# Kernel tuning notes

Measured on AMD Instinct MI355X. Metric: run time of the kernel, lower is better.

## Reference

```python
import jax, jax.numpy as jnp
import numpy as np

B, T, I, H, O, F = 256, 2048, 64, 256, 64, 16
NUM_LAYERS = 2


def setup_inputs() -> dict:
    key = jax.random.key(0)
    ks = jax.random.split(key, 12)
    s = 1.0 / np.sqrt(H)  # PyTorch RNN/Linear init scale
    u = lambda k, shp: jax.random.uniform(k, shp, jnp.float32, -s, s)
    return {
        "x": jax.random.normal(ks[0], (B, T, I), jnp.float32),
        "hidden": jnp.zeros((NUM_LAYERS, B, H), jnp.float32),
        "W_ih0": u(ks[1], (H, I)),
        "W_hh0": u(ks[2], (H, H)),
        "b_ih0": u(ks[3], (H,)),
        "b_hh0": u(ks[4], (H,)),
        "W_ih1": u(ks[5], (H, H)),
        "W_hh1": u(ks[6], (H, H)),
        "b_ih1": u(ks[7], (H,)),
        "b_hh1": u(ks[8], (H,)),
        "fc_W": u(ks[9], (O, H)),
        "fc_b": u(ks[10], (O,)),
        "future_timesegments": F,
    }


def _rnn_layer(xs, h0, W_ih, W_hh, b_ih, b_hh):
    # xs: [T, B, in_dim]; h0: [B, H]
    # Precompute input contribution for all timesteps (one big GEMM),
    # then scan only the sequential recurrence h@W_hh^T + tanh.
    pre = jnp.einsum('tbi,hi->tbh', xs, W_ih) + b_ih + b_hh  # [T, B, H]

    def step(h, p_t):
        h_new = jnp.tanh(p_t + h @ W_hh.T)
        return h_new, h_new

    h_T, ys = jax.lax.scan(step, h0, pre)
    return ys, h_T  # ys: [T, B, H]


def reference(x, hidden, W_ih0, W_hh0, b_ih0, b_hh0,
              W_ih1, W_hh1, b_ih1, b_hh1, fc_W, fc_b,
              future_timesegments):
    xs = jnp.swapaxes(x, 0, 1)  # [T, B, I] (batch_first -> time major)
    ys0, h0 = _rnn_layer(xs, hidden[0], W_ih0, W_hh0, b_ih0, b_hh0)
    ys1, h1 = _rnn_layer(ys0, hidden[1], W_ih1, W_hh1, b_ih1, b_hh1)
    # out[:, -F:, :] in batch-first layout
    tail = jnp.swapaxes(ys1[-future_timesegments:], 0, 1)  # [B, F, H]
    out = tail @ fc_W.T + fc_b  # [B, F, O]
    new_hidden = jnp.stack([h0, h1])  # [num_layers, B, H]
    return out, new_hidden
```

## Files before the change

### kernel.cpp

```cpp
#include <hip/hip_runtime.h>

#define BB 256
#define TT 2048
#define II 64
#define HH 256
#define OO 64
#define FF 16


#define BUFSZ 1280
#define BUF0 0
#define BUF1 BUFSZ
#define H1OFF 576
#define XOFF 1152
#define HSL 144
#define XSL 32
#define TAILOFF (2 * BUFSZ)
#define LDSBYTES (TAILOFF + FF * HH * 2)

typedef _Float16 h8 __attribute__((ext_vector_type(8)));

__device__ __forceinline__ void adot(float& acc, int hv, int wv) {
  asm("v_dot2_f32_f16 %0, %1, %2, %0" : "+v"(acc) : "v"(hv), "v"(wv));
}

__device__ __forceinline__ float fast_tanh(float z) {
  float e = __builtin_amdgcn_exp2f(z * 2.885390081777927f);
  return 1.0f - 2.0f * __builtin_amdgcn_rcpf(e + 1.0f);
}

__device__ __forceinline__ int pk2i(const float* p) {
  union { _Float16 h[2]; int i; } u;
  u.h[0] = (_Float16)p[0]; u.h[1] = (_Float16)p[1];
  return u.i;
}

template <int CTRL>
__device__ __forceinline__ float dpp_add(float v) {
  union { float f; int i; } a, r;
  a.f = v;
  r.i = __builtin_amdgcn_update_dpp(0, a.i, CTRL, 0xF, 0xF, true);
  return v + r.f;
}

#define RNN_STEP(T, RB, WB)                                                    \
  {                                                                            \
    float xn = 0.f;                                                            \
    if ((tid & 7) == 0) {                                                      \
      int tn = (T) + 1 < TT ? (T) + 1 : (T);                                   \
      xn = xrow[(size_t)tn * II + xi];                                         \
    }                                                                          \
    float a00 = 0.f, a01 = 0.f, a10 = 0.f, a11 = 0.f;                          \
    _Pragma("unroll") for (int c = 0; c < 2; ++c) {                            \
      const int4 v = *(const int4*)(xaddr + (RB) + c * 16);                    \
      adot(a00, v.x, w0x[0][4 * c + 0]); adot(a00, v.y, w0x[0][4 * c + 1]);    \
      adot(a00, v.z, w0x[0][4 * c + 2]); adot(a00, v.w, w0x[0][4 * c + 3]);    \
      adot(a01, v.x, w0x[1][4 * c + 0]); adot(a01, v.y, w0x[1][4 * c + 1]);    \
      adot(a01, v.z, w0x[1][4 * c + 2]); adot(a01, v.w, w0x[1][4 * c + 3]);    \
    }                                                                          \
    _Pragma("unroll") for (int c = 0; c < 8; ++c) {                            \
      const int4 v = *(const int4*)(h0addr + (RB) + c * 16);                   \
      adot(a00, v.x, w0h[0][4 * c + 0]); adot(a00, v.y, w0h[0][4 * c + 1]);    \
      adot(a00, v.z, w0h[0][4 * c + 2]); adot(a00, v.w, w0h[0][4 * c + 3]);    \
      adot(a01, v.x, w0h[1][4 * c + 0]); adot(a01, v.y, w0h[1][4 * c + 1]);    \
      adot(a01, v.z, w0h[1][4 * c + 2]); adot(a01, v.w, w0h[1][4 * c + 3]);    \
      adot(a10, v.x, w1g[0][4 * c + 0]); adot(a10, v.y, w1g[0][4 * c + 1]);    \
      adot(a10, v.z, w1g[0][4 * c + 2]); adot(a10, v.w, w1g[0][4 * c + 3]);    \
      adot(a11, v.x, w1g[1][4 * c + 0]); adot(a11, v.y, w1g[1][4 * c + 1]);    \
      adot(a11, v.z, w1g[1][4 * c + 2]); adot(a11, v.w, w1g[1][4 * c + 3]);    \
    }                                                                          \
    _Pragma("unroll") for (int c = 0; c < 8; ++c) {                            \
      const int4 v = *(const int4*)(h0addr + (RB) + H1OFF + c * 16);           \
      adot(a10, v.x, w1h[0][4 * c + 0]); adot(a10, v.y, w1h[0][4 * c + 1]);    \
      adot(a10, v.z, w1h[0][4 * c + 2]); adot(a10, v.w, w1h[0][4 * c + 3]);    \
      adot(a11, v.x, w1h[1][4 * c + 0]); adot(a11, v.y, w1h[1][4 * c + 1]);    \
      adot(a11, v.z, w1h[1][4 * c + 2]); adot(a11, v.w, w1h[1][4 * c + 3]);    \
    }                                                                          \
    a00 = dpp_add<0xB1>(a00); a00 = dpp_add<0x4E>(a00);                        \
    a01 = dpp_add<0xB1>(a01); a01 = dpp_add<0x4E>(a01);                        \
    a10 = dpp_add<0xB1>(a10); a10 = dpp_add<0x4E>(a10);                        \
    a11 = dpp_add<0xB1>(a11); a11 = dpp_add<0x4E>(a11);                        \
    float v0 = (kg & 1) ? a01 : a00;                                           \
    float v1 = (kg & 1) ? a11 : a10;                                           \
    float hnew = fast_tanh((L ? v1 : v0) + mybias);                            \
    hlast = hnew;                                                              \
    if ((T) > 0 || L == 0) *(_Float16*)(waddr + (WB)) = (_Float16)hnew;        \
    if (L == 1 && (T) >= TT - FF + 1)                                          \
      *(_Float16*)(tailaddr + ((T) - (TT - FF + 1)) * (HH * 2)) =              \
          (_Float16)hnew;                                                      \
    if ((tid & 7) == 0)                                                        \
      *(_Float16*)(lb + (WB) + XOFF + (xi >> 4) * XSL + (xi & 15) * 2) =       \
          (_Float16)xn;                                                        \
    __syncthreads();                                                           \
  }

__global__ __attribute__((amdgpu_flat_work_group_size(512, 512),
                          amdgpu_waves_per_eu(2, 2)))
void rnn_fused(const float* __restrict__ x, const float* __restrict__ hidden,
               const float* __restrict__ Wih0, const float* __restrict__ Whh0,
               const float* __restrict__ bih0, const float* __restrict__ bhh0,
               const float* __restrict__ Wih1, const float* __restrict__ Whh1,
               const float* __restrict__ bih1, const float* __restrict__ bhh1,
               const float* __restrict__ fcW, const float* __restrict__ fcb,
               float* __restrict__ out)
{
  const int tid = threadIdx.x;
  const int b = blockIdx.x;
  const int lane = tid & 63;
  const int kg = lane & 3;
  const int rg = tid >> 2;
  const int j0 = rg * 2;
  const int L = kg >> 1;
  const int cj = j0 + (kg & 1);
  const int xi = tid >> 3;

  __shared__ __align__(16) char lds[LDSBYTES];
  char* lb = (char*)lds;

  int w0x[2][8], w0h[2][32], w1g[2][32], w1h[2][32];
#pragma unroll
  for (int r = 0; r < 2; ++r) {
    const float* p0 = Wih0 + (size_t)(j0 + r) * II + kg * 16;
#pragma unroll
    for (int m = 0; m < 8; ++m) w0x[r][m] = pk2i(p0 + 2 * m);
    const float* p1 = Whh0 + (size_t)(j0 + r) * HH + kg * 64;
#pragma unroll
    for (int m = 0; m < 32; ++m) w0h[r][m] = pk2i(p1 + 2 * m);
    const float* p2 = Wih1 + (size_t)(j0 + r) * HH + kg * 64;
#pragma unroll
    for (int m = 0; m < 32; ++m) w1g[r][m] = pk2i(p2 + 2 * m);
    const float* p3 = Whh1 + (size_t)(j0 + r) * HH + kg * 64;
#pragma unroll
    for (int m = 0; m < 32; ++m) w1h[r][m] = pk2i(p3 + 2 * m);
  }
#pragma unroll
  for (int r = 0; r < 2; ++r) {
#pragma unroll
    for (int m = 0; m < 8; ++m) asm volatile("" : "+v"(w0x[r][m]));
#pragma unroll
    for (int m = 0; m < 32; ++m) {
      asm volatile("" : "+v"(w0h[r][m]));
      asm volatile("" : "+v"(w1g[r][m]));
      asm volatile("" : "+v"(w1h[r][m]));
    }
  }
  float mybias = L ? (bih1[cj] + bhh1[cj]) : (bih0[cj] + bhh0[cj]);
  asm volatile("" : "+v"(mybias));

  const char* h0addr = lb + kg * HSL;
  const char* xaddr = lb + XOFF + kg * XSL;
  char* waddr = lb + (L ? H1OFF : 0) + (cj >> 6) * HSL + (cj & 63) * 2;
  char* tailaddr = lb + TAILOFF + cj * 2;

  if (tid < HH) {
    char* p = lb + (tid >> 6) * HSL + (tid & 63) * 2;
    _Float16 h0v = (_Float16)hidden[(size_t)b * HH + tid];
    _Float16 h1v = (_Float16)hidden[(size_t)(BB + b) * HH + tid];
    *(_Float16*)(p + BUF0) = h0v;
    *(_Float16*)(p + BUF0 + H1OFF) = h1v;
    *(_Float16*)(p + BUF1 + H1OFF) = h1v;
  }
  const float* xrow = x + (size_t)b * TT * II;
  if (tid < II)
    *(_Float16*)(lb + BUF0 + XOFF + (tid >> 4) * XSL + (tid & 15) * 2) =
        (_Float16)xrow[tid];
  float hlast = 0.f, h1last = 0.f;
  __syncthreads();

#pragma unroll 1
  for (int t = 0; t < TT; t += 2) {
    RNN_STEP(t, BUF0, BUF1)
    RNN_STEP(t + 1, BUF1, BUF0)
  }

  {
    float a10 = 0.f, a11 = 0.f;
#pragma unroll
    for (int c = 0; c < 8; ++c) {
      const int4 v = *(const int4*)(h0addr + BUF0 + c * 16);
      adot(a10, v.x, w1g[0][4 * c + 0]); adot(a10, v.y, w1g[0][4 * c + 1]);
      adot(a10, v.z, w1g[0][4 * c + 2]); adot(a10, v.w, w1g[0][4 * c + 3]);
      adot(a11, v.x, w1g[1][4 * c + 0]); adot(a11, v.y, w1g[1][4 * c + 1]);
      adot(a11, v.z, w1g[1][4 * c + 2]); adot(a11, v.w, w1g[1][4 * c + 3]);
    }
#pragma unroll
    for (int c = 0; c < 8; ++c) {
      const int4 v = *(const int4*)(h0addr + BUF0 + H1OFF + c * 16);
      adot(a10, v.x, w1h[0][4 * c + 0]); adot(a10, v.y, w1h[0][4 * c + 1]);
      adot(a10, v.z, w1h[0][4 * c + 2]); adot(a10, v.w, w1h[0][4 * c + 3]);
      adot(a11, v.x, w1h[1][4 * c + 0]); adot(a11, v.y, w1h[1][4 * c + 1]);
      adot(a11, v.z, w1h[1][4 * c + 2]); adot(a11, v.w, w1h[1][4 * c + 3]);
    }
    a10 = dpp_add<0xB1>(a10); a10 = dpp_add<0x4E>(a10);
    a11 = dpp_add<0xB1>(a11); a11 = dpp_add<0x4E>(a11);
    float v1 = (kg & 1) ? a11 : a10;
    float h1e = fast_tanh(v1 + mybias);
    h1last = h1e;
    if (L == 1) *(_Float16*)(tailaddr + (FF - 1) * (HH * 2)) = (_Float16)h1e;
  }
  __syncthreads();

  if (L == 0) out[BB * FF * OO + (size_t)b * HH + cj] = hlast;
  else        out[BB * FF * OO + (size_t)(BB + b) * HH + cj] = h1last;

  const int o = tid & 63;
  const int fg = tid >> 6;
  const _Float16* tp = (const _Float16*)(lb + TAILOFF);
  float acc0 = 0.f, acc1 = 0.f;
  const float* wrow = fcW + o * HH;
  for (int c = 0; c < HH / 8; ++c) {
    float wv[8];
#pragma unroll
    for (int k = 0; k < 8; ++k) wv[k] = wrow[8 * c + k];
    h8 q0 = *(const h8*)(tp + (2 * fg) * HH + 8 * c);
    h8 q1 = *(const h8*)(tp + (2 * fg + 1) * HH + 8 * c);
#pragma unroll
    for (int e = 0; e < 8; ++e) {
      acc0 += (float)q0[e] * wv[e];
      acc1 += (float)q1[e] * wv[e];
    }
  }
  const float bo = fcb[o];
  out[((size_t)b * FF + 2 * fg) * OO + o] = acc0 + bo;
  out[((size_t)b * FF + 2 * fg + 1) * OO + o] = acc1 + bo;
}

extern "C" void kernel_launch(void* const* d_in, const int* in_sizes, int n_in,
                              void* d_out, int out_size, void* d_ws, size_t ws_size,
                              hipStream_t stream) {
  (void)in_sizes; (void)n_in; (void)d_ws; (void)ws_size; (void)out_size;
  rnn_fused<<<dim3(BB), dim3(512), 0, stream>>>(
      (const float*)d_in[0],  (const float*)d_in[1],
      (const float*)d_in[2],  (const float*)d_in[3],
      (const float*)d_in[4],  (const float*)d_in[5],
      (const float*)d_in[6],  (const float*)d_in[7],
      (const float*)d_in[8],  (const float*)d_in[9],
      (const float*)d_in[10], (const float*)d_in[11],
      (float*)d_out);
}
```

Measured before the change: 3.146 ms.

## Split each hidden unit's dot products across eight lanes with 1024-thread blocks

Each row pair is now reduced by eight lanes instead of four, and the block doubles to 1024 threads. This halves the per-thread reduction length and the weight registers, with an extra DPP reduction step added. The intent is to shorten the serial critical path of each recurrence step and allow more waves per SIMD. In exchange, a 1024-thread barrier runs every step, and half the lanes compute redundant tanh values whose results are discarded.

```diff
diff --git a/kernel.cpp b/kernel.cpp
--- a/kernel.cpp
+++ b/kernel.cpp
@@ -8,13 +8,12 @@
 #define FF 16
 
 
-#define BUFSZ 1280
+#define BUFSZ 1408
 #define BUF0 0
 #define BUF1 BUFSZ
-#define H1OFF 576
-#define XOFF 1152
-#define HSL 144
-#define XSL 32
+#define H1OFF 640
+#define XOFF 1280
+#define HSL 80
 #define TAILOFF (2 * BUFSZ)
 #define LDSBYTES (TAILOFF + FF * HH * 2)
 
@@ -46,19 +45,19 @@
 #define RNN_STEP(T, RB, WB)                                                    \
   {                                                                            \
     float xn = 0.f;                                                            \
-    if ((tid & 7) == 0) {                                                      \
+    if ((tid & 15) == 0) {                                                     \
       int tn = (T) + 1 < TT ? (T) + 1 : (T);                                   \
       xn = xrow[(size_t)tn * II + xi];                                         \
     }                                                                          \
     float a00 = 0.f, a01 = 0.f, a10 = 0.f, a11 = 0.f;                          \
-    _Pragma("unroll") for (int c = 0; c < 2; ++c) {                            \
-      const int4 v = *(const int4*)(xaddr + (RB) + c * 16);                    \
-      adot(a00, v.x, w0x[0][4 * c + 0]); adot(a00, v.y, w0x[0][4 * c + 1]);    \
-      adot(a00, v.z, w0x[0][4 * c + 2]); adot(a00, v.w, w0x[0][4 * c + 3]);    \
-      adot(a01, v.x, w0x[1][4 * c + 0]); adot(a01, v.y, w0x[1][4 * c + 1]);    \
-      adot(a01, v.z, w0x[1][4 * c + 2]); adot(a01, v.w, w0x[1][4 * c + 3]);    \
-    }                                                                          \
-    _Pragma("unroll") for (int c = 0; c < 8; ++c) {                            \
+    {                                                                          \
+      const int4 xv = *(const int4*)(xaddr + (RB));                            \
+      adot(a00, xv.x, w0x[0][0]); adot(a00, xv.y, w0x[0][1]);                  \
+      adot(a00, xv.z, w0x[0][2]); adot(a00, xv.w, w0x[0][3]);                  \
+      adot(a01, xv.x, w0x[1][0]); adot(a01, xv.y, w0x[1][1]);                  \
+      adot(a01, xv.z, w0x[1][2]); adot(a01, xv.w, w0x[1][3]);                  \
+    }                                                                          \
+    _Pragma("unroll") for (int c = 0; c < 4; ++c) {                            \
       const int4 v = *(const int4*)(h0addr + (RB) + c * 16);                   \
       adot(a00, v.x, w0h[0][4 * c + 0]); adot(a00, v.y, w0h[0][4 * c + 1]);    \
       adot(a00, v.z, w0h[0][4 * c + 2]); adot(a00, v.w, w0h[0][4 * c + 3]);    \
@@ -69,7 +68,7 @@
       adot(a11, v.x, w1g[1][4 * c + 0]); adot(a11, v.y, w1g[1][4 * c + 1]);    \
       adot(a11, v.z, w1g[1][4 * c + 2]); adot(a11, v.w, w1g[1][4 * c + 3]);    \
     }                                                                          \
-    _Pragma("unroll") for (int c = 0; c < 8; ++c) {                            \
+    _Pragma("unroll") for (int c = 0; c < 4; ++c) {                            \
       const int4 v = *(const int4*)(h0addr + (RB) + H1OFF + c * 16);           \
       adot(a10, v.x, w1h[0][4 * c + 0]); adot(a10, v.y, w1h[0][4 * c + 1]);    \
       adot(a10, v.z, w1h[0][4 * c + 2]); adot(a10, v.w, w1h[0][4 * c + 3]);    \
@@ -77,25 +76,31 @@
       adot(a11, v.z, w1h[1][4 * c + 2]); adot(a11, v.w, w1h[1][4 * c + 3]);    \
     }                                                                          \
     a00 = dpp_add<0xB1>(a00); a00 = dpp_add<0x4E>(a00);                        \
+    a00 = dpp_add<0x141>(a00);                                                 \
     a01 = dpp_add<0xB1>(a01); a01 = dpp_add<0x4E>(a01);                        \
+    a01 = dpp_add<0x141>(a01);                                                 \
     a10 = dpp_add<0xB1>(a10); a10 = dpp_add<0x4E>(a10);                        \
+    a10 = dpp_add<0x141>(a10);                                                 \
     a11 = dpp_add<0xB1>(a11); a11 = dpp_add<0x4E>(a11);                        \
-    float v0 = (kg & 1) ? a01 : a00;                                           \
-    float v1 = (kg & 1) ? a11 : a10;                                           \
-    float hnew = fast_tanh((L ? v1 : v0) + mybias);                            \
-    hlast = hnew;                                                              \
-    if ((T) > 0 || L == 0) *(_Float16*)(waddr + (WB)) = (_Float16)hnew;        \
-    if (L == 1 && (T) >= TT - FF + 1)                                          \
-      *(_Float16*)(tailaddr + ((T) - (TT - FF + 1)) * (HH * 2)) =              \
-          (_Float16)hnew;                                                      \
-    if ((tid & 7) == 0)                                                        \
-      *(_Float16*)(lb + (WB) + XOFF + (xi >> 4) * XSL + (xi & 15) * 2) =       \
+    a11 = dpp_add<0x141>(a11);                                                 \
+    float vA = (kg & 1) ? a01 : a00;                                           \
+    float vB = (kg & 1) ? a11 : a10;                                           \
+    float hnew = fast_tanh(((kg & 2) ? vB : vA) + mybias);                     \
+    if (kg < 4) {                                                              \
+      hlast = hnew;                                                            \
+      if ((T) > 0 || kg < 2) *(_Float16*)(waddr + (WB)) = (_Float16)hnew;      \
+      if (kg >= 2 && (T) >= TT - FF + 1)                                       \
+        *(_Float16*)(tailaddr + ((T) - (TT - FF + 1)) * (HH * 2)) =            \
+            (_Float16)hnew;                                                    \
+    }                                                                          \
+    if ((tid & 15) == 0)                                                       \
+      *(_Float16*)(lb + (WB) + XOFF + (xi >> 3) * 16 + (xi & 7) * 2) =         \
           (_Float16)xn;                                                        \
     __syncthreads();                                                           \
   }
 
-__global__ __attribute__((amdgpu_flat_work_group_size(512, 512),
-                          amdgpu_waves_per_eu(2, 2)))
+__global__ __attribute__((amdgpu_flat_work_group_size(1024, 1024),
+                          amdgpu_waves_per_eu(4, 4)))
 void rnn_fused(const float* __restrict__ x, const float* __restrict__ hidden,
                const float* __restrict__ Wih0, const float* __restrict__ Whh0,
                const float* __restrict__ bih0, const float* __restrict__ bhh0,
@@ -107,53 +112,52 @@
   const int tid = threadIdx.x;
   const int b = blockIdx.x;
   const int lane = tid & 63;
-  const int kg = lane & 3;
-  const int rg = tid >> 2;
-  const int j0 = rg * 2;
-  const int L = kg >> 1;
-  const int cj = j0 + (kg & 1);
-  const int xi = tid >> 3;
+  const int kg = lane & 7;
+  const int r0 = (tid >> 3) * 2;
+  const int cj = r0 + (kg & 1);
+  const int xi = tid >> 4;
 
   __shared__ __align__(16) char lds[LDSBYTES];
   char* lb = (char*)lds;
 
-  int w0x[2][8], w0h[2][32], w1g[2][32], w1h[2][32];
+  int w0x[2][4], w0h[2][16], w1g[2][16], w1h[2][16];
 #pragma unroll
   for (int r = 0; r < 2; ++r) {
-    const float* p0 = Wih0 + (size_t)(j0 + r) * II + kg * 16;
-#pragma unroll
-    for (int m = 0; m < 8; ++m) w0x[r][m] = pk2i(p0 + 2 * m);
-    const float* p1 = Whh0 + (size_t)(j0 + r) * HH + kg * 64;
-#pragma unroll
-    for (int m = 0; m < 32; ++m) w0h[r][m] = pk2i(p1 + 2 * m);
-    const float* p2 = Wih1 + (size_t)(j0 + r) * HH + kg * 64;
-#pragma unroll
-    for (int m = 0; m < 32; ++m) w1g[r][m] = pk2i(p2 + 2 * m);
-    const float* p3 = Whh1 + (size_t)(j0 + r) * HH + kg * 64;
-#pragma unroll
-    for (int m = 0; m < 32; ++m) w1h[r][m] = pk2i(p3 + 2 * m);
+    const float* p0 = Wih0 + (size_t)(r0 + r) * II + kg * 8;
+#pragma unroll
+    for (int m = 0; m < 4; ++m) w0x[r][m] = pk2i(p0 + 2 * m);
+    const float* p1 = Whh0 + (size_t)(r0 + r) * HH + kg * 32;
+#pragma unroll
+    for (int m = 0; m < 16; ++m) w0h[r][m] = pk2i(p1 + 2 * m);
+    const float* p2 = Wih1 + (size_t)(r0 + r) * HH + kg * 32;
+#pragma unroll
+    for (int m = 0; m < 16; ++m) w1g[r][m] = pk2i(p2 + 2 * m);
+    const float* p3 = Whh1 + (size_t)(r0 + r) * HH + kg * 32;
+#pragma unroll
+    for (int m = 0; m < 16; ++m) w1h[r][m] = pk2i(p3 + 2 * m);
   }
 #pragma unroll
   for (int r = 0; r < 2; ++r) {
 #pragma unroll
-    for (int m = 0; m < 8; ++m) asm volatile("" : "+v"(w0x[r][m]));
-#pragma unroll
-    for (int m = 0; m < 32; ++m) {
+    for (int m = 0; m < 4; ++m) asm volatile("" : "+v"(w0x[r][m]));
+#pragma unroll
+    for (int m = 0; m < 16; ++m) {
       asm volatile("" : "+v"(w0h[r][m]));
       asm volatile("" : "+v"(w1g[r][m]));
       asm volatile("" : "+v"(w1h[r][m]));
     }
   }
-  float mybias = L ? (bih1[cj] + bhh1[cj]) : (bih0[cj] + bhh0[cj]);
+  const int Lc = (kg >> 1) & 1;
+  float mybias = Lc ? (bih1[cj] + bhh1[cj]) : (bih0[cj] + bhh0[cj]);
   asm volatile("" : "+v"(mybias));
 
   const char* h0addr = lb + kg * HSL;
-  const char* xaddr = lb + XOFF + kg * XSL;
-  char* waddr = lb + (L ? H1OFF : 0) + (cj >> 6) * HSL + (cj & 63) * 2;
+  const char* xaddr = lb + XOFF + kg * 16;
+  char* waddr = lb + (Lc ? H1OFF : 0) + (cj >> 5) * HSL + (cj & 31) * 2;
   char* tailaddr = lb + TAILOFF + cj * 2;
 
   if (tid < HH) {
-    char* p = lb + (tid >> 6) * HSL + (tid & 63) * 2;
+    char* p = lb + (tid >> 5) * HSL + (tid & 31) * 2;
     _Float16 h0v = (_Float16)hidden[(size_t)b * HH + tid];
     _Float16 h1v = (_Float16)hidden[(size_t)(BB + b) * HH + tid];
     *(_Float16*)(p + BUF0) = h0v;
@@ -162,9 +166,9 @@
   }
   const float* xrow = x + (size_t)b * TT * II;
   if (tid < II)
-    *(_Float16*)(lb + BUF0 + XOFF + (tid >> 4) * XSL + (tid & 15) * 2) =
+    *(_Float16*)(lb + BUF0 + XOFF + (tid >> 3) * 16 + (tid & 7) * 2) =
         (_Float16)xrow[tid];
-  float hlast = 0.f, h1last = 0.f;
+  float hlast = 0.f;
   __syncthreads();
 
 #pragma unroll 1
@@ -176,7 +180,7 @@
   {
     float a10 = 0.f, a11 = 0.f;
 #pragma unroll
-    for (int c = 0; c < 8; ++c) {
+    for (int c = 0; c < 4; ++c) {
       const int4 v = *(const int4*)(h0addr + BUF0 + c * 16);
       adot(a10, v.x, w1g[0][4 * c + 0]); adot(a10, v.y, w1g[0][4 * c + 1]);
       adot(a10, v.z, w1g[0][4 * c + 2]); adot(a10, v.w, w1g[0][4 * c + 3]);
@@ -184,7 +188,7 @@
       adot(a11, v.z, w1g[1][4 * c + 2]); adot(a11, v.w, w1g[1][4 * c + 3]);
     }
 #pragma unroll
-    for (int c = 0; c < 8; ++c) {
+    for (int c = 0; c < 4; ++c) {
       const int4 v = *(const int4*)(h0addr + BUF0 + H1OFF + c * 16);
       adot(a10, v.x, w1h[0][4 * c + 0]); adot(a10, v.y, w1h[0][4 * c + 1]);
       adot(a10, v.z, w1h[0][4 * c + 2]); adot(a10, v.w, w1h[0][4 * c + 3]);
@@ -192,44 +196,41 @@
       adot(a11, v.z, w1h[1][4 * c + 2]); adot(a11, v.w, w1h[1][4 * c + 3]);
     }
     a10 = dpp_add<0xB1>(a10); a10 = dpp_add<0x4E>(a10);
+    a10 = dpp_add<0x141>(a10);
     a11 = dpp_add<0xB1>(a11); a11 = dpp_add<0x4E>(a11);
-    float v1 = (kg & 1) ? a11 : a10;
-    float h1e = fast_tanh(v1 + mybias);
-    h1last = h1e;
-    if (L == 1) *(_Float16*)(tailaddr + (FF - 1) * (HH * 2)) = (_Float16)h1e;
+    a11 = dpp_add<0x141>(a11);
+    float h1e = fast_tanh(((kg & 1) ? a11 : a10) + mybias);
+    if (kg == 2 || kg == 3) {
+      hlast = h1e;
+      *(_Float16*)(tailaddr + (FF - 1) * (HH * 2)) = (_Float16)h1e;
+    }
   }
   __syncthreads();
 
-  if (L == 0) out[BB * FF * OO + (size_t)b * HH + cj] = hlast;
-  else        out[BB * FF * OO + (size_t)(BB + b) * HH + cj] = h1last;
+  if (kg < 2)      out[BB * FF * OO + (size_t)b * HH + cj] = hlast;
+  else if (kg < 4) out[BB * FF * OO + (size_t)(BB + b) * HH + cj] = hlast;
 
   const int o = tid & 63;
-  const int fg = tid >> 6;
-  const _Float16* tp = (const _Float16*)(lb + TAILOFF);
-  float acc0 = 0.f, acc1 = 0.f;
+  const int f = tid >> 6;
+  const _Float16* trow = (const _Float16*)(lb + TAILOFF) + f * HH;
+  float acc = 0.f;
   const float* wrow = fcW + o * HH;
   for (int c = 0; c < HH / 8; ++c) {
     float wv[8];
 #pragma unroll
     for (int k = 0; k < 8; ++k) wv[k] = wrow[8 * c + k];
-    h8 q0 = *(const h8*)(tp + (2 * fg) * HH + 8 * c);
-    h8 q1 = *(const h8*)(tp + (2 * fg + 1) * HH + 8 * c);
-#pragma unroll
-    for (int e = 0; e < 8; ++e) {
-      acc0 += (float)q0[e] * wv[e];
-      acc1 += (float)q1[e] * wv[e];
-    }
-  }
-  const float bo = fcb[o];
-  out[((size_t)b * FF + 2 * fg) * OO + o] = acc0 + bo;
-  out[((size_t)b * FF + 2 * fg + 1) * OO + o] = acc1 + bo;
+    h8 q = *(const h8*)(trow + 8 * c);
+#pragma unroll
+    for (int e = 0; e < 8; ++e) acc += (float)q[e] * wv[e];
+  }
+  out[((size_t)b * FF + f) * OO + o] = acc + fcb[o];
 }
 
 extern "C" void kernel_launch(void* const* d_in, const int* in_sizes, int n_in,
                               void* d_out, int out_size, void* d_ws, size_t ws_size,
                               hipStream_t stream) {
   (void)in_sizes; (void)n_in; (void)d_ws; (void)ws_size; (void)out_size;
-  rnn_fused<<<dim3(BB), dim3(512), 0, stream>>>(
+  rnn_fused<<<dim3(BB), dim3(1024), 0, stream>>>(
       (const float*)d_in[0],  (const float*)d_in[1],
       (const float*)d_in[2],  (const float*)d_in[3],
       (const float*)d_in[4],  (const float*)d_in[5],
```

After: 3.707 ms. 17.8% more time.
